# Performance work log

Hardware: AMD Instinct MI355X
Metric: run time of the kernel (lower is better)

The kernel has to match this reference:

```python
import jax, jax.numpy as jnp
import numpy as np

EPS = 1e-5
NUM_GN_GROUPS = 32


def setup_inputs() -> dict:
    key = jax.random.key(0)
    k1, k2, k3 = jax.random.split(key, 3)
    B, C, N, G = 2, 256, 4096, 8
    c = C // G
    return {
        "points": jax.random.normal(k1, (B, C, N), dtype=jnp.float32),
        "conv_w": jax.random.normal(k2, (G, c, c), dtype=jnp.float32) / np.sqrt(c),
        "conv_b": jax.random.normal(k3, (C,), dtype=jnp.float32) * 0.02,
        "gn_w": jnp.ones((C,), dtype=jnp.float32),
        "gn_b": jnp.zeros((C,), dtype=jnp.float32),
    }


def reference(points, conv_w, conv_b, gn_w, gn_b):
    B, C, N = points.shape
    G = conv_w.shape[0]
    c = C // G  # channels per attention group
    identity = points

    # grouped 1x1 conv: per-group [c,c] matmul + bias
    x = points.reshape(B, G, c, N)
    x = jnp.einsum('gij,bgjn->bgin', conv_w, x) + conv_b.reshape(1, G, c, 1)

    # attention[b,g,n,m] = sum_i x[b,g,i,n] * x[b,g,i,m] / sqrt(c)
    scale = 1.0 / np.sqrt(c).astype(np.float32)
    attn = jnp.einsum('bgin,bgim->bgnm', x, x) * scale
    # softmax over dim=2 (the query/row N axis -- non-standard)
    attn = jax.nn.softmax(attn, axis=2)

    # ELU-gated second matmul: [B,G,c,N] @ [B,G,N,N] -> [B,G,c,N]
    x = jnp.einsum('bgcn,bgnm->bgcm', jax.nn.elu(x), attn)

    # channel shuffle: [B,G,c,N] -> [B,c,G,N] -> [B,C,N]
    x = x.transpose(0, 2, 1, 3).reshape(B, C, N)
    x = x + identity

    # GroupNorm(32 groups) over (channels-in-group, N)
    xg = x.reshape(B, NUM_GN_GROUPS, C // NUM_GN_GROUPS, N)
    mean = xg.mean(axis=(2, 3), keepdims=True)
    var = xg.var(axis=(2, 3), keepdims=True)
    xg = (xg - mean) * jax.lax.rsqrt(var + EPS)
    x = xg.reshape(B, C, N)
    return x * gn_w.reshape(1, C, 1) + gn_b.reshape(1, C, 1)
```

## Files before the change

kernel.cpp:

```cpp
#include <hip/hip_runtime.h>

typedef __attribute__((ext_vector_type(8))) short bf16x8;
typedef __attribute__((ext_vector_type(4))) short bf16x4;
typedef __attribute__((ext_vector_type(4))) float f32x4;

#if __has_builtin(__builtin_amdgcn_exp2f)
#define EXP2(x) __builtin_amdgcn_exp2f(x)
#else
#define EXP2(x) exp2f(x)
#endif

__device__ __forceinline__ unsigned short f2bf(float f) {
    union { float f; unsigned int u; } v; v.f = f;
    unsigned int r = v.u + 0x7fffu + ((v.u >> 16) & 1u);
    return (unsigned short)(r >> 16);
}

__device__ __forceinline__ float asf(unsigned int u) {
    union { unsigned int u; float f; } v; v.u = u; return v.f;
}

#define QK_PRESCALE 0.50500983f

__global__ __launch_bounds__(256) void conv_kernel(
    const float* __restrict__ points, const float* __restrict__ conv_w,
    const float* __restrict__ conv_b,
    unsigned short* __restrict__ xqT, unsigned short* __restrict__ xv)
{
    __shared__ float w[1024];
    const int h  = blockIdx.x >> 4;
    const int nc = blockIdx.x & 15;
    const int g  = h & 7;
    const int tid = threadIdx.x;
    const float* wg = conv_w + g * 1024;
    for (int k = tid; k < 1024; k += 256) w[k] = wg[k];
    __syncthreads();
    const int n = nc * 256 + tid;
    const float* p = points + (size_t)h * 32 * 4096 + n;
    float pv[32];
#pragma unroll
    for (int j = 0; j < 32; ++j) pv[j] = p[(size_t)j * 4096];
    float out[32];
#pragma unroll
    for (int i = 0; i < 32; ++i) {
        float acc = conv_b[g * 32 + i];
        const float4* w4 = (const float4*)(w + i * 32);
#pragma unroll
        for (int j4 = 0; j4 < 8; ++j4) {
            float4 ww = w4[j4];
            acc += ww.x * pv[j4 * 4]     + ww.y * pv[j4 * 4 + 1]
                 + ww.z * pv[j4 * 4 + 2] + ww.w * pv[j4 * 4 + 3];
        }
        out[i] = acc;
    }
    unsigned short tq[32];
#pragma unroll
    for (int i = 0; i < 32; ++i) tq[i] = f2bf(out[i] * QK_PRESCALE);
    bf16x8* dst = (bf16x8*)(xqT + ((size_t)h * 4096 + n) * 32);
#pragma unroll
    for (int t = 0; t < 4; ++t) dst[t] = ((bf16x8*)tq)[t];
#pragma unroll
    for (int i = 0; i < 32; ++i) {
        float x = out[i];
        float e = x > 0.f ? x : (__expf(x) - 1.f);
        xv[((size_t)h * 32 + i) * 4096 + n] = f2bf(e);
    }
}

#define KSTR 40
#define VSTR 136
#define PSTR 72

#if __has_builtin(__builtin_amdgcn_cvt_pk_bf16_f32)
typedef __attribute__((ext_vector_type(2))) __bf16 bf16x2v;
__device__ __forceinline__ bf16x4 exp_pack(f32x4 sc, float& lsum) {
    float e0 = EXP2(sc[0]), e1 = EXP2(sc[1]);
    float e2 = EXP2(sc[2]), e3 = EXP2(sc[3]);
    lsum += (e0 + e1) + (e2 + e3);
    union { bf16x2v v[2]; bf16x4 s; } u;
    u.v[0] = __builtin_amdgcn_cvt_pk_bf16_f32(e0, e1);
    u.v[1] = __builtin_amdgcn_cvt_pk_bf16_f32(e2, e3);
    return u.s;
}
#else
__device__ __forceinline__ bf16x4 exp_pack(f32x4 sc, float& lsum) {
    union { float f; unsigned int u; } e0, e1, e2, e3;
    e0.f = EXP2(sc[0]); e1.f = EXP2(sc[1]); e2.f = EXP2(sc[2]); e3.f = EXP2(sc[3]);
    unsigned int t0 = e0.u & 0xffff0000u, t1 = e1.u & 0xffff0000u;
    unsigned int t2 = e2.u & 0xffff0000u, t3 = e3.u & 0xffff0000u;
    lsum += (asf(t0) + asf(t1)) + (asf(t2) + asf(t3));
    union { unsigned int d[2]; bf16x4 v; } pk;
    pk.d[0] = (t0 >> 16) | t1;
    pk.d[1] = (t2 >> 16) | t3;
    return pk.v;
}
#endif

__global__ __launch_bounds__(256) void attn_kernel(
    const unsigned short* __restrict__ xqT,
    const unsigned short* __restrict__ xv,
    const float* __restrict__ points,
    float* __restrict__ z)
{
    __shared__ unsigned short Kt[128 * KSTR];
    __shared__ unsigned short Vt[32 * VSTR];
    __shared__ unsigned short Pl[4][16 * PSTR];

    const int h  = blockIdx.y;
    const int b = h >> 3, g = h & 7;
    const int tid = threadIdx.x;
    const int wv = tid >> 6, lane = tid & 63;
    const int quad = lane >> 4, l15 = lane & 15;

    const int m = blockIdx.x * 64 + wv * 16 + l15;

    const unsigned short* kbase = xqT + (size_t)h * 4096 * 32;
    const unsigned short* vbase = xv  + (size_t)h * 32 * 4096;

    const bf16x8 qfrag = *(const bf16x8*)(kbase + (size_t)m * 32 + quad * 8);

    f32x4 acc0 = {0.f, 0.f, 0.f, 0.f};
    f32x4 acc1 = {0.f, 0.f, 0.f, 0.f};
    float lsum = 0.f;

    const int kr = tid >> 2, kc = (tid & 3) * 8;
    const int vi = tid >> 3, vn = (tid & 7) * 8;

    unsigned short* pw = &Pl[wv][0];

    const unsigned short* kptrA = kbase + (size_t)kr * 32 + kc;
    const unsigned short* kptrB = kbase + (size_t)(64 + kr) * 32 + kc;
    const unsigned short* vptr  = vbase + (size_t)vi * 4096 + vn;
    bf16x8 ka = *(const bf16x8*)kptrA;
    bf16x8 kb = *(const bf16x8*)kptrB;
    bf16x8 va = *(const bf16x8*)vptr;
    bf16x8 vb = *(const bf16x8*)(vptr + 64);

    for (int n0 = 0; n0 < 4096; n0 += 128) {
        __syncthreads();
        *(bf16x8*)(Kt + kr * KSTR + kc)        = ka;
        *(bf16x8*)(Kt + (kr + 64) * KSTR + kc) = kb;
        *(bf16x8*)(Vt + vi * VSTR + vn)        = va;
        *(bf16x8*)(Vt + vi * VSTR + vn + 64)   = vb;
        __syncthreads();

        if (n0 + 128 < 4096) {
            kptrA += 128 * 32; kptrB += 128 * 32; vptr += 128;
            ka = *(const bf16x8*)kptrA;
            kb = *(const bf16x8*)kptrB;
            va = *(const bf16x8*)vptr;
            vb = *(const bf16x8*)(vptr + 64);
        }

#pragma unroll
        for (int sub = 0; sub < 2; ++sub) {
#pragma unroll
            for (int s = 0; s < 4; ++s) {
                bf16x8 kf = *(const bf16x8*)(
                    Kt + (sub * 64 + s * 16 + l15) * KSTR + quad * 8);
                f32x4 sc = __builtin_amdgcn_mfma_f32_16x16x32_bf16(
                    kf, qfrag, (f32x4){0.f, 0.f, 0.f, 0.f}, 0, 0, 0);
                bf16x4 pk = exp_pack(sc, lsum);
                *(bf16x4*)(pw + l15 * PSTR + s * 16 + quad * 4) = pk;
            }
#pragma unroll
            for (int ng = 0; ng < 2; ++ng) {
                bf16x8 pf = *(const bf16x8*)(pw + l15 * PSTR + ng * 32 + quad * 8);
                const int col = sub * 64 + ng * 32 + quad * 8;
                bf16x8 v0 = *(const bf16x8*)(Vt + l15 * VSTR + col);
                bf16x8 v1 = *(const bf16x8*)(Vt + (16 + l15) * VSTR + col);
                acc0 = __builtin_amdgcn_mfma_f32_16x16x32_bf16(v0, pf, acc0, 0, 0, 0);
                acc1 = __builtin_amdgcn_mfma_f32_16x16x32_bf16(v1, pf, acc1, 0, 0, 0);
            }
        }
    }

    lsum += __shfl_xor(lsum, 16, 64);
    lsum += __shfl_xor(lsum, 32, 64);
    const float inv = 1.f / lsum;

    const float* pb = points + (size_t)b * 256 * 4096;
    float* zb = z + (size_t)b * 256 * 4096;
#pragma unroll
    for (int half = 0; half < 2; ++half) {
        f32x4 a = half ? acc1 : acc0;
#pragma unroll
        for (int r = 0; r < 4; ++r) {
            int i = half * 16 + quad * 4 + r;
            size_t off = (size_t)(i * 8 + g) * 4096 + m;
            zb[off] = a[r] * inv + pb[off];
        }
    }
}

__global__ __launch_bounds__(256) void gn_stats(const float* __restrict__ z,
                                                float* __restrict__ pstats)
{
    const int blk = blockIdx.x;
    const int tid = threadIdx.x;
    const float4* p = (const float4*)(z + (size_t)blk * 8192);
    float s = 0.f, ss = 0.f;
    for (int k = tid; k < 2048; k += 256) {
        float4 v = p[k];
        s  += v.x + v.y + v.z + v.w;
        ss += v.x * v.x + v.y * v.y + v.z * v.z + v.w * v.w;
    }
#pragma unroll
    for (int off = 32; off > 0; off >>= 1) {
        s  += __shfl_down(s, off, 64);
        ss += __shfl_down(ss, off, 64);
    }
    __shared__ float red[8];
    const int w = tid >> 6;
    if ((tid & 63) == 0) { red[w * 2] = s; red[w * 2 + 1] = ss; }
    __syncthreads();
    if (tid == 0) {
        s  = red[0] + red[2] + red[4] + red[6];
        ss = red[1] + red[3] + red[5] + red[7];
        pstats[blk * 2]     = s;
        pstats[blk * 2 + 1] = ss;
    }
}

__global__ __launch_bounds__(256) void gn_apply(float* __restrict__ z,
                                                const float* __restrict__ pstats,
                                                const float* __restrict__ gw,
                                                const float* __restrict__ gb)
{
    const int idx = blockIdx.x * 256 + threadIdx.x;
    float4* p = (float4*)z;
    float4 v = p[idx];
    const int chg = idx >> 10;
    const int grp = chg >> 3;
    const int ch  = chg & 255;
    const float4 s4  = *(const float4*)(pstats + grp * 8);
    const float4 s4b = *(const float4*)(pstats + grp * 8 + 4);
    const float s  = s4.x + s4.z + s4b.x + s4b.z;
    const float ss = s4.y + s4.w + s4b.y + s4b.w;
    const float mean = s * (1.f / 32768.f);
    const float var  = ss * (1.f / 32768.f) - mean * mean;
    const float rstd = rsqrtf(var + 1e-5f);
    const float w  = gw[ch] * rstd;
    const float bb = gb[ch] - mean * w;
    v.x = v.x * w + bb; v.y = v.y * w + bb;
    v.z = v.z * w + bb; v.w = v.w * w + bb;
    p[idx] = v;
}

extern "C" void kernel_launch(void* const* d_in, const int* in_sizes, int n_in,
                              void* d_out, int out_size, void* d_ws, size_t ws_size,
                              hipStream_t stream)
{
    const float* points = (const float*)d_in[0];
    const float* conv_w = (const float*)d_in[1];
    const float* conv_b = (const float*)d_in[2];
    const float* gn_w   = (const float*)d_in[3];
    const float* gn_b   = (const float*)d_in[4];
    float* out = (float*)d_out;
    char* ws = (char*)d_ws;
    unsigned short* xqT = (unsigned short*)ws;
    unsigned short* xv  = (unsigned short*)(ws + (size_t)4 * 1024 * 1024);
    float* pstats = (float*)(ws + (size_t)8 * 1024 * 1024);

    conv_kernel<<<256, 256, 0, stream>>>(points, conv_w, conv_b, xqT, xv);
    attn_kernel<<<dim3(64, 16), 256, 0, stream>>>(xqT, xv, points, out);
    gn_stats<<<256, 256, 0, stream>>>(out, pstats);
    gn_apply<<<2048, 256, 0, stream>>>(out, pstats, gn_w, gn_b);
}
```

Measured before the change: 161.1 us.

## Load K fragments straight to registers, double-buffer, and split conv across more blocks

The attention kernel no longer stages K tiles through shared memory. Each lane loads its MFMA K fragments directly from global memory into two register buffers, with the loop unrolled by two so the next chunk prefetches while the current one computes. A launch bound of 4 blocks per SM is added. The conv kernel is split four ways over output channels (1024 blocks), which adds parallelism and reduces registers per thread but makes each block reload the same point columns. The cost is more global K traffic and register pressure, in exchange for fewer LDS writes and reads.

```diff
diff --git a/kernel.cpp b/kernel.cpp
--- a/kernel.cpp
+++ b/kernel.cpp
@@ -28,21 +28,23 @@
     unsigned short* __restrict__ xqT, unsigned short* __restrict__ xv)
 {
     __shared__ float w[1024];
-    const int h  = blockIdx.x >> 4;
-    const int nc = blockIdx.x & 15;
+    const int h  = blockIdx.x >> 6;
+    const int nc = blockIdx.x & 63;
     const int g  = h & 7;
     const int tid = threadIdx.x;
     const float* wg = conv_w + g * 1024;
     for (int k = tid; k < 1024; k += 256) w[k] = wg[k];
     __syncthreads();
-    const int n = nc * 256 + tid;
+    const int n  = nc * 64 + (tid & 63);
+    const int ig = tid >> 6;
     const float* p = points + (size_t)h * 32 * 4096 + n;
     float pv[32];
 #pragma unroll
     for (int j = 0; j < 32; ++j) pv[j] = p[(size_t)j * 4096];
-    float out[32];
-#pragma unroll
-    for (int i = 0; i < 32; ++i) {
+    float out[8];
+#pragma unroll
+    for (int ii = 0; ii < 8; ++ii) {
+        const int i = ig * 8 + ii;
         float acc = conv_b[g * 32 + i];
         const float4* w4 = (const float4*)(w + i * 32);
 #pragma unroll
@@ -51,23 +53,20 @@
             acc += ww.x * pv[j4 * 4]     + ww.y * pv[j4 * 4 + 1]
                  + ww.z * pv[j4 * 4 + 2] + ww.w * pv[j4 * 4 + 3];
         }
-        out[i] = acc;
-    }
-    unsigned short tq[32];
-#pragma unroll
-    for (int i = 0; i < 32; ++i) tq[i] = f2bf(out[i] * QK_PRESCALE);
-    bf16x8* dst = (bf16x8*)(xqT + ((size_t)h * 4096 + n) * 32);
-#pragma unroll
-    for (int t = 0; t < 4; ++t) dst[t] = ((bf16x8*)tq)[t];
-#pragma unroll
-    for (int i = 0; i < 32; ++i) {
-        float x = out[i];
+        out[ii] = acc;
+    }
+    unsigned short tq[8];
+#pragma unroll
+    for (int ii = 0; ii < 8; ++ii) tq[ii] = f2bf(out[ii] * QK_PRESCALE);
+    *(bf16x8*)(xqT + ((size_t)h * 4096 + n) * 32 + ig * 8) = *(bf16x8*)tq;
+#pragma unroll
+    for (int ii = 0; ii < 8; ++ii) {
+        float x = out[ii];
         float e = x > 0.f ? x : (__expf(x) - 1.f);
-        xv[((size_t)h * 32 + i) * 4096 + n] = f2bf(e);
-    }
-}
-
-#define KSTR 40
+        xv[((size_t)h * 32 + ig * 8 + ii) * 4096 + n] = f2bf(e);
+    }
+}
+
 #define VSTR 136
 #define PSTR 72
 
@@ -96,13 +95,49 @@
 }
 #endif
 
-__global__ __launch_bounds__(256) void attn_kernel(
+#define CHUNK(C0, KU, KP)                                                      \
+    {                                                                          \
+        __syncthreads();                                                       \
+        *(bf16x8*)(Vt + vi * VSTR + vn)      = va;                             \
+        *(bf16x8*)(Vt + vi * VSTR + vn + 64) = vb;                             \
+        __syncthreads();                                                       \
+        const int pfb = ((C0) + 128) & 4095;                                   \
+        va = *(const bf16x8*)(vbase + (size_t)vi * 4096 + pfb + vn);           \
+        vb = *(const bf16x8*)(vbase + (size_t)vi * 4096 + pfb + vn + 64);      \
+        _Pragma("unroll")                                                      \
+        for (int s8 = 0; s8 < 8; ++s8)                                         \
+            KP[s8] = *(const bf16x8*)(kfp + (size_t)(pfb + s8 * 16) * 32);     \
+        _Pragma("unroll")                                                      \
+        for (int sub = 0; sub < 2; ++sub) {                                    \
+            _Pragma("unroll")                                                  \
+            for (int s = 0; s < 4; ++s) {                                      \
+                f32x4 sc = __builtin_amdgcn_mfma_f32_16x16x32_bf16(            \
+                    KU[sub * 4 + s], qfrag, (f32x4){0.f, 0.f, 0.f, 0.f},       \
+                    0, 0, 0);                                                  \
+                bf16x4 pk = exp_pack(sc, lsum);                                \
+                *(bf16x4*)(pw + l15 * PSTR + s * 16 + quad * 4) = pk;          \
+            }                                                                  \
+            _Pragma("unroll")                                                  \
+            for (int ng = 0; ng < 2; ++ng) {                                   \
+                bf16x8 pfrag = *(const bf16x8*)(pw + l15 * PSTR + ng * 32 +    \
+                                                quad * 8);                     \
+                const int col = sub * 64 + ng * 32 + quad * 8;                 \
+                bf16x8 v0 = *(const bf16x8*)(Vt + l15 * VSTR + col);           \
+                bf16x8 v1 = *(const bf16x8*)(Vt + (16 + l15) * VSTR + col);    \
+                acc0 = __builtin_amdgcn_mfma_f32_16x16x32_bf16(v0, pfrag,      \
+                                                               acc0, 0, 0, 0); \
+                acc1 = __builtin_amdgcn_mfma_f32_16x16x32_bf16(v1, pfrag,      \
+                                                               acc1, 0, 0, 0); \
+            }                                                                  \
+        }                                                                      \
+    }
+
+__global__ __launch_bounds__(256, 4) void attn_kernel(
     const unsigned short* __restrict__ xqT,
     const unsigned short* __restrict__ xv,
     const float* __restrict__ points,
     float* __restrict__ z)
 {
-    __shared__ unsigned short Kt[128 * KSTR];
     __shared__ unsigned short Vt[32 * VSTR];
     __shared__ unsigned short Pl[4][16 * PSTR];
 
@@ -123,56 +158,23 @@
     f32x4 acc1 = {0.f, 0.f, 0.f, 0.f};
     float lsum = 0.f;
 
-    const int kr = tid >> 2, kc = (tid & 3) * 8;
     const int vi = tid >> 3, vn = (tid & 7) * 8;
-
     unsigned short* pw = &Pl[wv][0];
 
-    const unsigned short* kptrA = kbase + (size_t)kr * 32 + kc;
-    const unsigned short* kptrB = kbase + (size_t)(64 + kr) * 32 + kc;
-    const unsigned short* vptr  = vbase + (size_t)vi * 4096 + vn;
-    bf16x8 ka = *(const bf16x8*)kptrA;
-    bf16x8 kb = *(const bf16x8*)kptrB;
+    const unsigned short* kfp = kbase + (size_t)l15 * 32 + quad * 8;
+
+    const unsigned short* vptr = vbase + (size_t)vi * 4096 + vn;
     bf16x8 va = *(const bf16x8*)vptr;
     bf16x8 vb = *(const bf16x8*)(vptr + 64);
 
-    for (int n0 = 0; n0 < 4096; n0 += 128) {
-        __syncthreads();
-        *(bf16x8*)(Kt + kr * KSTR + kc)        = ka;
-        *(bf16x8*)(Kt + (kr + 64) * KSTR + kc) = kb;
-        *(bf16x8*)(Vt + vi * VSTR + vn)        = va;
-        *(bf16x8*)(Vt + vi * VSTR + vn + 64)   = vb;
-        __syncthreads();
-
-        if (n0 + 128 < 4096) {
-            kptrA += 128 * 32; kptrB += 128 * 32; vptr += 128;
-            ka = *(const bf16x8*)kptrA;
-            kb = *(const bf16x8*)kptrB;
-            va = *(const bf16x8*)vptr;
-            vb = *(const bf16x8*)(vptr + 64);
-        }
-
-#pragma unroll
-        for (int sub = 0; sub < 2; ++sub) {
-#pragma unroll
-            for (int s = 0; s < 4; ++s) {
-                bf16x8 kf = *(const bf16x8*)(
-                    Kt + (sub * 64 + s * 16 + l15) * KSTR + quad * 8);
-                f32x4 sc = __builtin_amdgcn_mfma_f32_16x16x32_bf16(
-                    kf, qfrag, (f32x4){0.f, 0.f, 0.f, 0.f}, 0, 0, 0);
-                bf16x4 pk = exp_pack(sc, lsum);
-                *(bf16x4*)(pw + l15 * PSTR + s * 16 + quad * 4) = pk;
-            }
-#pragma unroll
-            for (int ng = 0; ng < 2; ++ng) {
-                bf16x8 pf = *(const bf16x8*)(pw + l15 * PSTR + ng * 32 + quad * 8);
-                const int col = sub * 64 + ng * 32 + quad * 8;
-                bf16x8 v0 = *(const bf16x8*)(Vt + l15 * VSTR + col);
-                bf16x8 v1 = *(const bf16x8*)(Vt + (16 + l15) * VSTR + col);
-                acc0 = __builtin_amdgcn_mfma_f32_16x16x32_bf16(v0, pf, acc0, 0, 0, 0);
-                acc1 = __builtin_amdgcn_mfma_f32_16x16x32_bf16(v1, pf, acc1, 0, 0, 0);
-            }
-        }
+    bf16x8 kA[8], kB[8];
+#pragma unroll
+    for (int s8 = 0; s8 < 8; ++s8)
+        kA[s8] = *(const bf16x8*)(kfp + (size_t)(s8 * 16) * 32);
+
+    for (int n0 = 0; n0 < 4096; n0 += 256) {
+        CHUNK(n0,       kA, kB);
+        CHUNK(n0 + 128, kB, kA);
     }
 
     lsum += __shfl_xor(lsum, 16, 64);
@@ -262,7 +264,7 @@
     unsigned short* xv  = (unsigned short*)(ws + (size_t)4 * 1024 * 1024);
     float* pstats = (float*)(ws + (size_t)8 * 1024 * 1024);
 
-    conv_kernel<<<256, 256, 0, stream>>>(points, conv_w, conv_b, xqT, xv);
+    conv_kernel<<<1024, 256, 0, stream>>>(points, conv_w, conv_b, xqT, xv);
     attn_kernel<<<dim3(64, 16), 256, 0, stream>>>(xqT, xv, points, out);
     gn_stats<<<256, 256, 0, stream>>>(out, pstats);
     gn_apply<<<2048, 256, 0, stream>>>(out, pstats, gn_w, gn_b);
```

New measurement: 152.9 us. 5.1% less time.
